# Kernel optimization log

Hardware: AMD Instinct MI355X
Metric: run time of the kernel (lower is better)

The kernel has to match this reference:

```python
import jax, jax.numpy as jnp
import numpy as np

N_HEAD = 8
D_MODEL = 128  # per-head dim == d_model in this 'interpretable' MHA
B, S = 2, 2048
LN_EPS = 1e-3  # keras LayerNormalization default epsilon


def setup_inputs() -> dict:
    key = jax.random.key(0)
    ks = jax.random.split(key, 8)
    sc = 1.0 / np.sqrt(D_MODEL)
    q = jax.random.normal(ks[0], (B, S, D_MODEL), jnp.float32)
    k = jax.random.normal(ks[1], (B, S, D_MODEL), jnp.float32)
    v = jax.random.normal(ks[2], (B, S, D_MODEL), jnp.float32)
    # multiplicative causal mask (lower-triangular ones), broadcast over B,H
    mask = jnp.tril(jnp.ones((S, S), jnp.float32))[None, None, :, :]
    Wq = jax.random.normal(ks[3], (D_MODEL, N_HEAD * D_MODEL), jnp.float32) * sc
    Wk = jax.random.normal(ks[4], (D_MODEL, N_HEAD * D_MODEL), jnp.float32) * sc
    Wv = jax.random.normal(ks[5], (D_MODEL, N_HEAD * D_MODEL), jnp.float32) * sc
    Wo = jax.random.normal(ks[6], (N_HEAD * D_MODEL, D_MODEL), jnp.float32) * sc
    gamma = jnp.ones((D_MODEL,), jnp.float32)
    beta = jnp.zeros((D_MODEL,), jnp.float32)
    return {"q": q, "k": k, "v": v, "mask": mask, "Wq": Wq, "Wk": Wk,
            "Wv": Wv, "Wo": Wo, "gamma": gamma, "beta": beta}


def reference(q, k, v, mask, Wq, Wk, Wv, Wo, gamma, beta):
    b = q.shape[0]
    # projections -> [B, H, S, D]
    def split_heads(x):
        return x.reshape(b, -1, N_HEAD, D_MODEL).transpose(0, 2, 1, 3)
    qs = split_heads(q @ Wq)
    ks_ = split_heads(k @ Wk)
    vs = split_heads(v @ Wv)
    scores = jnp.einsum('bhqd,bhkd->bhqk', qs, ks_) / jnp.sqrt(jnp.float32(D_MODEL))
    scores = scores * mask  # multiplicative mask (NOT additive -inf)
    attn = jax.nn.softmax(scores, axis=-1)
    # dropout layers are identity at inference
    out = jnp.einsum('bhqk,bhkd->bhqd', attn, vs)
    out = out.transpose(0, 2, 1, 3).reshape(b, -1, N_HEAD * D_MODEL)
    out = out @ Wo
    # keras LayerNorm (axis=-1, eps=1e-3)
    mu = jnp.mean(out, axis=-1, keepdims=True)
    var = jnp.var(out, axis=-1, keepdims=True)
    out = (out - mu) * jax.lax.rsqrt(var + LN_EPS) * gamma + beta
    return out
```

## Files before the change

### kernel.cpp

```cpp
#include <hip/hip_runtime.h>
#include <math.h>

#define B 2
#define S 2048
#define H 8
#define D 128
#define DM 1024
#define BH 16

typedef unsigned short u16;
typedef __attribute__((ext_vector_type(8))) short bf16x8;
typedef __attribute__((ext_vector_type(8))) unsigned short u16x8;
typedef __attribute__((ext_vector_type(4))) float f32x4;

__device__ __forceinline__ float bf2f(u16 x) {
    union { unsigned u; float f; } c; c.u = ((unsigned)x) << 16; return c.f;
}
__device__ __forceinline__ u16 f2bf(float f) {
    union { unsigned u; float f; } c; c.f = f;
    unsigned u = c.u; u += 0x7fffu + ((u >> 16) & 1u);
    return (u16)(u >> 16);
}
__device__ __forceinline__ u16 ftr(float f) {
    union { unsigned u; float f; } c; c.f = f;
    return (u16)(c.u >> 16);
}

#define MFMA16(a, b, c) __builtin_amdgcn_mfma_f32_16x16x32_bf16((a), (b), (c), 0, 0, 0)

__global__ __launch_bounds__(256) void prep_kernel(
    const float* __restrict__ Wq, const float* __restrict__ Wk, const float* __restrict__ Wv,
    const float* __restrict__ Wo, u16* __restrict__ WT, u16* __restrict__ WoT)
{
    __shared__ __align__(16) u16 Wl[128][132];
    int tid = threadIdx.x, by = blockIdx.x;
    if (by < 16) {
        int k0 = by * 64;
#pragma unroll
        for (int i = 0; i < 8; i++) {
            int e = i * 256 + tid; int kk = e >> 5, n4 = e & 31;
            float4 w4 = *(const float4*)&Wo[(size_t)(k0 + kk) * D + n4 * 4];
            ushort4 p; p.x = ftr(w4.x); p.y = ftr(w4.y); p.z = ftr(w4.z); p.w = ftr(w4.w);
            *(ushort4*)&Wl[kk][n4 * 4] = p;
        }
        __syncthreads();
#pragma unroll
        for (int i = 0; i < 4; i++) {
            int e = i * 256 + tid; int n = e >> 3, ko = e & 7;
            u16x8 g;
#pragma unroll
            for (int j = 0; j < 8; j++) g[j] = Wl[ko * 8 + j][n];
            *(u16x8*)&WoT[(size_t)n * DM + k0 + ko * 8] = g;
        }
    } else {
        int tile = by - 16;
        int t = tile >> 3, h = tile & 7;
        const float* W = (t == 0) ? Wq : (t == 1) ? Wk : Wv;
        int col0 = h * 128;
#pragma unroll
        for (int i = 0; i < 16; i++) {
            int e = i * 256 + tid; int kk = e >> 5, n4 = e & 31;
            float4 w4 = *(const float4*)&W[(size_t)kk * DM + col0 + n4 * 4];
            ushort4 p; p.x = ftr(w4.x); p.y = ftr(w4.y); p.z = ftr(w4.z); p.w = ftr(w4.w);
            *(ushort4*)&Wl[kk][n4 * 4] = p;
        }
        __syncthreads();
        u16* WTt = WT + (size_t)tile * (128 * 128);
#pragma unroll
        for (int i = 0; i < 8; i++) {
            int e = i * 256 + tid; int n = e >> 4, ko = e & 15;
            u16x8 g;
#pragma unroll
            for (int j = 0; j < 8; j++) g[j] = Wl[ko * 8 + j][n];
            *(u16x8*)&WTt[(size_t)n * 128 + ko * 8] = g;
        }
    }
}

__global__ __launch_bounds__(256) void proj_kernel(
    const float* __restrict__ q, const float* __restrict__ k, const float* __restrict__ v,
    const u16* __restrict__ WT,
    u16* __restrict__ Qo, u16* __restrict__ Ko, u16* __restrict__ VTo,
    float* __restrict__ Csum)
{
    __shared__ __align__(16) u16 Xs[128][136];
    int tid = threadIdx.x;
    int m0 = blockIdx.x * 128;
    int by = blockIdx.y;
    int t = by >> 3;
    int h = by & 7;
    const float* X = (t == 0) ? q : (t == 1) ? k : v;
    const u16* WTt = WT + (size_t)(t * 8 + h) * (128 * 128);

#pragma unroll
    for (int i = 0; i < 16; i++) {
        int e = i * 256 + tid; int r = e >> 5, c4 = e & 31;
        float4 x4 = *(const float4*)&X[(size_t)(m0 + r) * D + c4 * 4];
        ushort4 p; p.x = ftr(x4.x); p.y = ftr(x4.y); p.z = ftr(x4.z); p.w = ftr(x4.w);
        *(ushort4*)&Xs[r][c4 * 4] = p;
    }
    __syncthreads();

    int w = tid >> 6, lane = tid & 63, quad = lane >> 4, ln = lane & 15;
    bf16x8 aX[2][4];
#pragma unroll
    for (int rf = 0; rf < 2; rf++)
#pragma unroll
        for (int ks = 0; ks < 4; ks++)
            aX[rf][ks] = *(const bf16x8*)&Xs[w * 32 + rf * 16 + ln][ks * 32 + quad * 8];

    f32x4 zero = {0.f, 0.f, 0.f, 0.f};
    f32x4 acc[2][8];
#pragma unroll
    for (int rf = 0; rf < 2; rf++)
#pragma unroll
        for (int nt = 0; nt < 8; nt++) acc[rf][nt] = zero;

#pragma unroll
    for (int ks = 0; ks < 4; ks++) {
        bf16x8 bW[8];
#pragma unroll
        for (int nt = 0; nt < 8; nt++)
            bW[nt] = *(const bf16x8*)&WTt[(size_t)(nt * 16 + ln) * 128 + ks * 32 + quad * 8];
#pragma unroll
        for (int nt = 0; nt < 8; nt++) {
            acc[0][nt] = MFMA16(aX[0][ks], bW[nt], acc[0][nt]);
            acc[1][nt] = MFMA16(aX[1][ks], bW[nt], acc[1][nt]);
        }
    }

    int bb = m0 >> 11, ss0 = m0 & 2047;
    int bh = bb * 8 + h;
    if (t < 2) {
        u16* O = (t == 0) ? Qo : Ko;
#pragma unroll
        for (int rf = 0; rf < 2; rf++)
#pragma unroll
            for (int nt = 0; nt < 8; nt++)
#pragma unroll
                for (int r = 0; r < 4; r++) {
                    int ss = ss0 + w * 32 + rf * 16 + quad * 4 + r;
                    O[((size_t)bh * S + ss) * D + nt * 16 + ln] = f2bf(acc[rf][nt][r]);
                }
    } else {
        __syncthreads();
        u16 (*Ct)[136] = Xs;
#pragma unroll
        for (int rf = 0; rf < 2; rf++)
#pragma unroll
            for (int nt = 0; nt < 8; nt++)
#pragma unroll
                for (int r = 0; r < 4; r++)
                    Ct[nt * 16 + ln][w * 32 + rf * 16 + quad * 4 + r] = f2bf(acc[rf][nt][r]);
        __syncthreads();
#pragma unroll
        for (int i = 0; i < 8; i++) {
            int e = i * 256 + tid; int dloc = e >> 4, s8 = e & 15;
            *(u16x8*)&VTo[((size_t)bh * D + dloc) * S + ss0 + s8 * 8] =
                *(const u16x8*)&Ct[dloc][s8 * 8];
        }
        {
            int d = tid >> 1, c = tid & 1;
            float s = 0.f;
#pragma unroll
            for (int i = 0; i < 8; i++) {
                u16x8 v8 = *(const u16x8*)&Ct[d][c * 64 + i * 8];
#pragma unroll
                for (int j = 0; j < 8; j++) s += bf2f(v8[j]);
            }
            Csum[((size_t)bh * 32 + (ss0 >> 6) + c) * D + d] = s;
        }
    }
}

__global__ __launch_bounds__(128) void scan_kernel(
    const float* __restrict__ Csum, float* __restrict__ SufT)
{
    int bh = blockIdx.x, d = threadIdx.x;
    float acc = 0.f;
    for (int c = 31; c >= 0; c--) {
        SufT[((size_t)bh * 32 + c) * D + d] = acc;
        acc += Csum[((size_t)bh * 32 + c) * D + d];
    }
}

__global__ __launch_bounds__(512, 2) void attn_kernel(
    const u16* __restrict__ Qb, const u16* __restrict__ Kb, const u16* __restrict__ VTg,
    const float* __restrict__ SufT, u16* __restrict__ HOb)
{
    __shared__ __align__(16) u16 Qs[2][64][136];
    __shared__ __align__(16) u16 Ks[128][136];
    __shared__ __align__(16) u16 Vt[128][136];
    __shared__ __align__(16) u16 Ps[2][64][136];
    __shared__ float Lred[2][4][64];

    int tid = threadIdx.x;
    int bx = blockIdx.x, bh = blockIdx.y;
    int nhi = (31 - bx) / 2 + 1, nlo = bx / 2 + 1;
    int w = tid >> 6, qt = w >> 2, wq = w & 3, lane = tid & 63, quad = lane >> 4, ln = lane & 15;
    int qb = qt ? bx : (31 - bx);
    int q0 = qb * 64;
    int nq = qt ? nlo : nhi;
    const u16* Qp  = Qb  + (size_t)bh * S * D;
    const u16* Kp  = Kb  + (size_t)bh * S * D;
    const u16* VTp = VTg + (size_t)bh * D * S;

#pragma unroll
    for (int i = 0; i < 4; i++) {
        int e = i * 512 + tid; int r2 = e >> 4, c8 = e & 15;
        int qtt = r2 >> 6, r = r2 & 63;
        int q0s = (qtt ? bx : (31 - bx)) * 64;
        *(u16x8*)&Qs[qtt][r][c8 * 8] = *(const u16x8*)&Qp[(size_t)(q0s + r) * D + c8 * 8];
    }
    __syncthreads();
    bf16x8 aQ[4][4];
#pragma unroll
    for (int rf = 0; rf < 4; rf++)
#pragma unroll
        for (int ks = 0; ks < 4; ks++)
            aQ[rf][ks] = *(const bf16x8*)&Qs[qt][rf * 16 + ln][ks * 32 + quad * 8];

    f32x4 zero = {0.f, 0.f, 0.f, 0.f};
    f32x4 accPV[4][2], acc_l[4];
#pragma unroll
    for (int rf = 0; rf < 4; rf++) { accPV[rf][0] = zero; accPV[rf][1] = zero; acc_l[rf] = zero; }
    bf16x8 bOnes;
#pragma unroll
    for (int j = 0; j < 8; j++) bOnes[j] = (short)0x3F80;
    const float scale = 0.08838834764831845f;

    for (int kt = 0; kt < nhi; kt++) {
        __syncthreads();
        int k0 = kt * 128;
#pragma unroll
        for (int i = 0; i < 4; i++) {
            int e = i * 512 + tid; int r = e >> 4, c8 = e & 15;
            *(u16x8*)&Ks[r][c8 * 8] = *(const u16x8*)&Kp[(size_t)(k0 + r) * D + c8 * 8];
        }
#pragma unroll
        for (int i = 0; i < 4; i++) {
            int e = i * 512 + tid; int dd = e >> 4, c8 = e & 15;
            *(u16x8*)&Vt[dd][c8 * 8] = *(const u16x8*)&VTp[(size_t)dd * S + k0 + c8 * 8];
        }
        __syncthreads();
        bool active = (qt == 0) || (kt < nlo);
        if (active) {
            f32x4 s[4][2];
#pragma unroll
            for (int rf = 0; rf < 4; rf++) { s[rf][0] = zero; s[rf][1] = zero; }
#pragma unroll
            for (int ks = 0; ks < 4; ks++) {
                bf16x8 b0 = *(const bf16x8*)&Ks[wq * 32 + ln][ks * 32 + quad * 8];
                bf16x8 b1 = *(const bf16x8*)&Ks[wq * 32 + 16 + ln][ks * 32 + quad * 8];
#pragma unroll
                for (int rf = 0; rf < 4; rf++) {
                    s[rf][0] = MFMA16(aQ[rf][ks], b0, s[rf][0]);
                    s[rf][1] = MFMA16(aQ[rf][ks], b1, s[rf][1]);
                }
            }
#pragma unroll
            for (int rf = 0; rf < 4; rf++)
#pragma unroll
                for (int ct = 0; ct < 2; ct++) {
                    int col = k0 + wq * 32 + ct * 16 + ln;
                    int rowb = q0 + rf * 16 + quad * 4;
#pragma unroll
                    for (int r = 0; r < 4; r++) {
                        float tv = (col <= rowb + r) ? s[rf][ct][r] : 0.f;
                        float p = __expf(tv * scale);
                        Ps[qt][rf * 16 + quad * 4 + r][wq * 32 + ct * 16 + ln] = f2bf(p);
                    }
                }
        }
        __syncthreads();
        if (active) {
#pragma unroll
            for (int ks = 0; ks < 4; ks++) {
                bf16x8 aP[4];
#pragma unroll
                for (int rf = 0; rf < 4; rf++)
                    aP[rf] = *(const bf16x8*)&Ps[qt][rf * 16 + ln][ks * 32 + quad * 8];
                bf16x8 v0 = *(const bf16x8*)&Vt[wq * 32 + ln][ks * 32 + quad * 8];
                bf16x8 v1 = *(const bf16x8*)&Vt[wq * 32 + 16 + ln][ks * 32 + quad * 8];
                if (ks == wq) {
#pragma unroll
                    for (int rf = 0; rf < 4; rf++) acc_l[rf] = MFMA16(aP[rf], bOnes, acc_l[rf]);
                }
#pragma unroll
                for (int rf = 0; rf < 4; rf++) {
                    accPV[rf][0] = MFMA16(aP[rf], v0, accPV[rf][0]);
                    accPV[rf][1] = MFMA16(aP[rf], v1, accPV[rf][1]);
                }
            }
        }
    }

    __syncthreads();
    if (ln == 0) {
#pragma unroll
        for (int rf = 0; rf < 4; rf++)
#pragma unroll
            for (int r = 0; r < 4; r++)
                Lred[qt][wq][rf * 16 + quad * 4 + r] = acc_l[rf][r];
    }
    __syncthreads();

    int scount = S - nq * 128;
    size_t sufb = (size_t)(bh * 32 + 2 * nq - 1) * D + wq * 32;
    float suf0 = SufT[sufb + ln];
    float suf1 = SufT[sufb + 16 + ln];
    int b = bh >> 3, h = bh & 7;
#pragma unroll
    for (int rf = 0; rf < 4; rf++)
#pragma unroll
        for (int r = 0; r < 4; r++) {
            int row = rf * 16 + quad * 4 + r;
            int srow = q0 + row;
            float l = Lred[qt][0][row] + Lred[qt][1][row] + Lred[qt][2][row] + Lred[qt][3][row]
                      + (float)scount;
            float inv = 1.f / l;
            size_t base = ((size_t)(b * S + srow)) * DM + h * D + wq * 32;
            HOb[base + ln]      = f2bf((accPV[rf][0][r] + suf0) * inv);
            HOb[base + 16 + ln] = f2bf((accPV[rf][1][r] + suf1) * inv);
        }
}

__global__ __launch_bounds__(256) void out_ln_kernel(
    const u16* __restrict__ HOb, const u16* __restrict__ WoT,
    const float* __restrict__ gamma, const float* __restrict__ beta,
    float* __restrict__ out)
{
    __shared__ __align__(16) u16 HOs[16][1048];
    __shared__ float Cs[16][132];
    int tid = threadIdx.x;
    int m0 = blockIdx.x * 16;
    int w = tid >> 6, lane = tid & 63, quad = lane >> 4, ln = lane & 15;
#pragma unroll
    for (int i = 0; i < 8; i++) {
        int e = i * 256 + tid; int r = e >> 7, c8 = e & 127;
        *(u16x8*)&HOs[r][c8 * 8] = *(const u16x8*)&HOb[(size_t)(m0 + r) * DM + c8 * 8];
    }
    __syncthreads();
    f32x4 zero = {0.f, 0.f, 0.f, 0.f};
    f32x4 acc[2] = {zero, zero};
#pragma unroll 4
    for (int ks = 0; ks < 32; ks++) {
        bf16x8 aH = *(const bf16x8*)&HOs[ln][ks * 32 + quad * 8];
        bf16x8 w0 = *(const bf16x8*)&WoT[(size_t)(w * 32 + ln) * DM + ks * 32 + quad * 8];
        bf16x8 w1 = *(const bf16x8*)&WoT[(size_t)(w * 32 + 16 + ln) * DM + ks * 32 + quad * 8];
        acc[0] = MFMA16(aH, w0, acc[0]);
        acc[1] = MFMA16(aH, w1, acc[1]);
    }
#pragma unroll
    for (int ct = 0; ct < 2; ct++)
#pragma unroll
        for (int r = 0; r < 4; r++)
            Cs[quad * 4 + r][w * 32 + ct * 16 + ln] = acc[ct][r];
    __syncthreads();

    int row = tid >> 4, t16 = tid & 15;
    float xv[8], sum = 0.f, sq = 0.f;
#pragma unroll
    for (int j = 0; j < 8; j++) {
        float x = Cs[row][t16 * 8 + j];
        xv[j] = x; sum += x; sq += x * x;
    }
#pragma unroll
    for (int off = 1; off < 16; off <<= 1) {
        sum += __shfl_xor(sum, off);
        sq  += __shfl_xor(sq, off);
    }
    float mu = sum * (1.f / 128.f);
    float var = sq * (1.f / 128.f) - mu * mu;
    float rstd = rsqrtf(var + 1e-3f);
    float o[8];
#pragma unroll
    for (int j = 0; j < 8; j++) {
        int c = t16 * 8 + j;
        o[j] = (xv[j] - mu) * rstd * gamma[c] + beta[c];
    }
    float* op = &out[(size_t)(m0 + row) * D + t16 * 8];
    *(float4*)&op[0] = *(float4*)&o[0];
    *(float4*)&op[4] = *(float4*)&o[4];
}

extern "C" void kernel_launch(void* const* d_in, const int* in_sizes, int n_in,
                              void* d_out, int out_size, void* d_ws, size_t ws_size,
                              hipStream_t stream)
{
    const float* q     = (const float*)d_in[0];
    const float* k     = (const float*)d_in[1];
    const float* v     = (const float*)d_in[2];
    const float* Wq    = (const float*)d_in[4];
    const float* Wk    = (const float*)d_in[5];
    const float* Wv    = (const float*)d_in[6];
    const float* Wo    = (const float*)d_in[7];
    const float* gamma = (const float*)d_in[8];
    const float* beta  = (const float*)d_in[9];

    u16* ws16 = (u16*)d_ws;
    u16* Qb  = ws16;
    u16* Kb  = ws16 + 4194304;
    u16* VT  = ws16 + 8388608;
    u16* HOb = ws16 + 12582912;
    u16* WoT = ws16 + 16777216;
    u16* WT  = ws16 + 16908288;
    float* Csum = (float*)((char*)d_ws + 35651584);
    float* SufT = (float*)((char*)d_ws + 35913728);

    prep_kernel<<<40, 256, 0, stream>>>(Wq, Wk, Wv, Wo, WT, WoT);
    proj_kernel<<<dim3(32, 24), 256, 0, stream>>>(q, k, v, WT, Qb, Kb, VT, Csum);
    scan_kernel<<<BH, 128, 0, stream>>>(Csum, SufT);
    attn_kernel<<<dim3(16, BH), 512, 0, stream>>>(Qb, Kb, VT, SufT, HOb);
    out_ln_kernel<<<256, 256, 0, stream>>>(HOb, WoT, gamma, beta, (float*)d_out);
}
```

Before: 165.4 us.

## Restructure attention to one 64-row query tile per block and drop scan kernel

The attention kernel now gives each block a single 64-row query tile with 4 waves of 16 rows and 64-key tiles. This replaces the paired high/low tile scheme that used 512 threads. The grid doubles to 512 blocks, each block loads only the key tiles it needs, and the suffix sum over masked value chunks is computed inline from Csum, which removes the separate scan kernel launch. The projection kernel stages the weight tile in LDS and writes Q/K through LDS with coalesced 16-byte stores. Costs are redundant suffix summation per thread and more K/V tile reloads across blocks.

```diff
diff --git a/kernel.cpp b/kernel.cpp
--- a/kernel.cpp
+++ b/kernel.cpp
@@ -84,6 +84,7 @@
     float* __restrict__ Csum)
 {
     __shared__ __align__(16) u16 Xs[128][136];
+    __shared__ __align__(16) u16 Ws[128][136];
     int tid = threadIdx.x;
     int m0 = blockIdx.x * 128;
     int by = blockIdx.y;
@@ -99,6 +100,11 @@
         ushort4 p; p.x = ftr(x4.x); p.y = ftr(x4.y); p.z = ftr(x4.z); p.w = ftr(x4.w);
         *(ushort4*)&Xs[r][c4 * 4] = p;
     }
+#pragma unroll
+    for (int i = 0; i < 8; i++) {
+        int e = i * 256 + tid; int n = e >> 4, c8 = e & 15;
+        *(u16x8*)&Ws[n][c8 * 8] = *(const u16x8*)&WTt[(size_t)n * 128 + c8 * 8];
+    }
     __syncthreads();
 
     int w = tid >> 6, lane = tid & 63, quad = lane >> 4, ln = lane & 15;
@@ -121,7 +127,7 @@
         bf16x8 bW[8];
 #pragma unroll
         for (int nt = 0; nt < 8; nt++)
-            bW[nt] = *(const bf16x8*)&WTt[(size_t)(nt * 16 + ln) * 128 + ks * 32 + quad * 8];
+            bW[nt] = *(const bf16x8*)&Ws[nt * 16 + ln][ks * 32 + quad * 8];
 #pragma unroll
         for (int nt = 0; nt < 8; nt++) {
             acc[0][nt] = MFMA16(aX[0][ks], bW[nt], acc[0][nt]);
@@ -131,6 +137,8 @@
 
     int bb = m0 >> 11, ss0 = m0 & 2047;
     int bh = bb * 8 + h;
+    __syncthreads();
+    u16 (*Ct)[136] = Xs;
     if (t < 2) {
         u16* O = (t == 0) ? Qo : Ko;
 #pragma unroll
@@ -138,13 +146,15 @@
 #pragma unroll
             for (int nt = 0; nt < 8; nt++)
 #pragma unroll
-                for (int r = 0; r < 4; r++) {
-                    int ss = ss0 + w * 32 + rf * 16 + quad * 4 + r;
-                    O[((size_t)bh * S + ss) * D + nt * 16 + ln] = f2bf(acc[rf][nt][r]);
-                }
+                for (int r = 0; r < 4; r++)
+                    Ct[w * 32 + rf * 16 + quad * 4 + r][nt * 16 + ln] = f2bf(acc[rf][nt][r]);
+        __syncthreads();
+#pragma unroll
+        for (int i = 0; i < 8; i++) {
+            int e = i * 256 + tid; int r = e >> 4, c8 = e & 15;
+            *(u16x8*)&O[((size_t)bh * S + ss0 + r) * D + c8 * 8] = *(const u16x8*)&Ct[r][c8 * 8];
+        }
     } else {
-        __syncthreads();
-        u16 (*Ct)[136] = Xs;
 #pragma unroll
         for (int rf = 0; rf < 2; rf++)
 #pragma unroll
@@ -173,156 +183,105 @@
     }
 }
 
-__global__ __launch_bounds__(128) void scan_kernel(
-    const float* __restrict__ Csum, float* __restrict__ SufT)
-{
-    int bh = blockIdx.x, d = threadIdx.x;
-    float acc = 0.f;
-    for (int c = 31; c >= 0; c--) {
-        SufT[((size_t)bh * 32 + c) * D + d] = acc;
-        acc += Csum[((size_t)bh * 32 + c) * D + d];
-    }
-}
-
-__global__ __launch_bounds__(512, 2) void attn_kernel(
+__global__ __launch_bounds__(256, 3) void attn_kernel(
     const u16* __restrict__ Qb, const u16* __restrict__ Kb, const u16* __restrict__ VTg,
-    const float* __restrict__ SufT, u16* __restrict__ HOb)
-{
-    __shared__ __align__(16) u16 Qs[2][64][136];
-    __shared__ __align__(16) u16 Ks[128][136];
-    __shared__ __align__(16) u16 Vt[128][136];
-    __shared__ __align__(16) u16 Ps[2][64][136];
-    __shared__ float Lred[2][4][64];
+    const float* __restrict__ Csum, u16* __restrict__ HOb)
+{
+    __shared__ __align__(16) u16 Ks[64][136];
+    __shared__ __align__(16) u16 Vt[128][72];
+    __shared__ __align__(16) u16 Ps[4][16][72];
 
     int tid = threadIdx.x;
-    int bx = blockIdx.x, bh = blockIdx.y;
-    int nhi = (31 - bx) / 2 + 1, nlo = bx / 2 + 1;
-    int w = tid >> 6, qt = w >> 2, wq = w & 3, lane = tid & 63, quad = lane >> 4, ln = lane & 15;
-    int qb = qt ? bx : (31 - bx);
+    int qb = 31 - blockIdx.x;
+    int bh = blockIdx.y;
     int q0 = qb * 64;
-    int nq = qt ? nlo : nhi;
+    int nt = (qb & ~1) + 2;
+    int w = tid >> 6, lane = tid & 63, quad = lane >> 4, ln = lane & 15;
     const u16* Qp  = Qb  + (size_t)bh * S * D;
     const u16* Kp  = Kb  + (size_t)bh * S * D;
     const u16* VTp = VTg + (size_t)bh * D * S;
 
-#pragma unroll
-    for (int i = 0; i < 4; i++) {
-        int e = i * 512 + tid; int r2 = e >> 4, c8 = e & 15;
-        int qtt = r2 >> 6, r = r2 & 63;
-        int q0s = (qtt ? bx : (31 - bx)) * 64;
-        *(u16x8*)&Qs[qtt][r][c8 * 8] = *(const u16x8*)&Qp[(size_t)(q0s + r) * D + c8 * 8];
-    }
-    __syncthreads();
-    bf16x8 aQ[4][4];
-#pragma unroll
-    for (int rf = 0; rf < 4; rf++)
-#pragma unroll
-        for (int ks = 0; ks < 4; ks++)
-            aQ[rf][ks] = *(const bf16x8*)&Qs[qt][rf * 16 + ln][ks * 32 + quad * 8];
+    bf16x8 aQ[4];
+    int qrow = q0 + w * 16 + ln;
+#pragma unroll
+    for (int ks = 0; ks < 4; ks++)
+        aQ[ks] = *(const bf16x8*)&Qp[(size_t)qrow * D + ks * 32 + quad * 8];
 
     f32x4 zero = {0.f, 0.f, 0.f, 0.f};
-    f32x4 accPV[4][2], acc_l[4];
-#pragma unroll
-    for (int rf = 0; rf < 4; rf++) { accPV[rf][0] = zero; accPV[rf][1] = zero; acc_l[rf] = zero; }
+    f32x4 accPV[8], acc_l[4];
+#pragma unroll
+    for (int jd = 0; jd < 8; jd++) accPV[jd] = zero;
+#pragma unroll
+    for (int g = 0; g < 4; g++) acc_l[g] = zero;
     bf16x8 bOnes;
 #pragma unroll
     for (int j = 0; j < 8; j++) bOnes[j] = (short)0x3F80;
     const float scale = 0.08838834764831845f;
 
-    for (int kt = 0; kt < nhi; kt++) {
-        __syncthreads();
-        int k0 = kt * 128;
+    for (int kt = 0; kt < nt; kt++) {
+        __syncthreads();
+        int k0 = kt * 64;
 #pragma unroll
         for (int i = 0; i < 4; i++) {
-            int e = i * 512 + tid; int r = e >> 4, c8 = e & 15;
+            int e = i * 256 + tid; int r = e >> 4, c8 = e & 15;
             *(u16x8*)&Ks[r][c8 * 8] = *(const u16x8*)&Kp[(size_t)(k0 + r) * D + c8 * 8];
         }
 #pragma unroll
         for (int i = 0; i < 4; i++) {
-            int e = i * 512 + tid; int dd = e >> 4, c8 = e & 15;
+            int e = i * 256 + tid; int dd = e >> 3, c8 = e & 7;
             *(u16x8*)&Vt[dd][c8 * 8] = *(const u16x8*)&VTp[(size_t)dd * S + k0 + c8 * 8];
         }
         __syncthreads();
-        bool active = (qt == 0) || (kt < nlo);
-        if (active) {
-            f32x4 s[4][2];
-#pragma unroll
-            for (int rf = 0; rf < 4; rf++) { s[rf][0] = zero; s[rf][1] = zero; }
+
+#pragma unroll
+        for (int ct = 0; ct < 4; ct++) {
+            f32x4 s = zero;
 #pragma unroll
             for (int ks = 0; ks < 4; ks++) {
-                bf16x8 b0 = *(const bf16x8*)&Ks[wq * 32 + ln][ks * 32 + quad * 8];
-                bf16x8 b1 = *(const bf16x8*)&Ks[wq * 32 + 16 + ln][ks * 32 + quad * 8];
-#pragma unroll
-                for (int rf = 0; rf < 4; rf++) {
-                    s[rf][0] = MFMA16(aQ[rf][ks], b0, s[rf][0]);
-                    s[rf][1] = MFMA16(aQ[rf][ks], b1, s[rf][1]);
-                }
+                bf16x8 bK = *(const bf16x8*)&Ks[ct * 16 + ln][ks * 32 + quad * 8];
+                s = MFMA16(aQ[ks], bK, s);
             }
-#pragma unroll
-            for (int rf = 0; rf < 4; rf++)
-#pragma unroll
-                for (int ct = 0; ct < 2; ct++) {
-                    int col = k0 + wq * 32 + ct * 16 + ln;
-                    int rowb = q0 + rf * 16 + quad * 4;
-#pragma unroll
-                    for (int r = 0; r < 4; r++) {
-                        float tv = (col <= rowb + r) ? s[rf][ct][r] : 0.f;
-                        float p = __expf(tv * scale);
-                        Ps[qt][rf * 16 + quad * 4 + r][wq * 32 + ct * 16 + ln] = f2bf(p);
-                    }
-                }
-        }
-        __syncthreads();
-        if (active) {
-#pragma unroll
-            for (int ks = 0; ks < 4; ks++) {
-                bf16x8 aP[4];
-#pragma unroll
-                for (int rf = 0; rf < 4; rf++)
-                    aP[rf] = *(const bf16x8*)&Ps[qt][rf * 16 + ln][ks * 32 + quad * 8];
-                bf16x8 v0 = *(const bf16x8*)&Vt[wq * 32 + ln][ks * 32 + quad * 8];
-                bf16x8 v1 = *(const bf16x8*)&Vt[wq * 32 + 16 + ln][ks * 32 + quad * 8];
-                if (ks == wq) {
-#pragma unroll
-                    for (int rf = 0; rf < 4; rf++) acc_l[rf] = MFMA16(aP[rf], bOnes, acc_l[rf]);
-                }
-#pragma unroll
-                for (int rf = 0; rf < 4; rf++) {
-                    accPV[rf][0] = MFMA16(aP[rf], v0, accPV[rf][0]);
-                    accPV[rf][1] = MFMA16(aP[rf], v1, accPV[rf][1]);
-                }
+            int col = k0 + ct * 16 + ln;
+            int rowb = q0 + w * 16 + quad * 4;
+#pragma unroll
+            for (int r = 0; r < 4; r++) {
+                float tv = (col <= rowb + r) ? s[r] : 0.f;
+                Ps[w][quad * 4 + r][ct * 16 + ln] = f2bf(__expf(tv * scale));
             }
         }
-    }
-
-    __syncthreads();
-    if (ln == 0) {
-#pragma unroll
-        for (int rf = 0; rf < 4; rf++)
-#pragma unroll
-            for (int r = 0; r < 4; r++)
-                Lred[qt][wq][rf * 16 + quad * 4 + r] = acc_l[rf][r];
-    }
-    __syncthreads();
-
-    int scount = S - nq * 128;
-    size_t sufb = (size_t)(bh * 32 + 2 * nq - 1) * D + wq * 32;
-    float suf0 = SufT[sufb + ln];
-    float suf1 = SufT[sufb + 16 + ln];
+#pragma unroll
+        for (int ks = 0; ks < 2; ks++) {
+            bf16x8 aP = *(const bf16x8*)&Ps[w][ln][ks * 32 + quad * 8];
+            int g = (2 * kt + ks) & 3;
+            acc_l[g] = MFMA16(aP, bOnes, acc_l[g]);
+#pragma unroll
+            for (int jd = 0; jd < 8; jd++) {
+                bf16x8 vf = *(const bf16x8*)&Vt[jd * 16 + ln][ks * 32 + quad * 8];
+                accPV[jd] = MFMA16(aP, vf, accPV[jd]);
+            }
+        }
+    }
+
+    float suf[8];
+#pragma unroll
+    for (int jd = 0; jd < 8; jd++) suf[jd] = 0.f;
+    for (int c = 31; c >= nt; c--) {
+        const float* cp = &Csum[((size_t)(bh * 32 + c)) * D + ln];
+#pragma unroll
+        for (int jd = 0; jd < 8; jd++) suf[jd] += cp[jd * 16];
+    }
+    int scount = S - nt * 64;
     int b = bh >> 3, h = bh & 7;
 #pragma unroll
-    for (int rf = 0; rf < 4; rf++)
-#pragma unroll
-        for (int r = 0; r < 4; r++) {
-            int row = rf * 16 + quad * 4 + r;
-            int srow = q0 + row;
-            float l = Lred[qt][0][row] + Lred[qt][1][row] + Lred[qt][2][row] + Lred[qt][3][row]
-                      + (float)scount;
-            float inv = 1.f / l;
-            size_t base = ((size_t)(b * S + srow)) * DM + h * D + wq * 32;
-            HOb[base + ln]      = f2bf((accPV[rf][0][r] + suf0) * inv);
-            HOb[base + 16 + ln] = f2bf((accPV[rf][1][r] + suf1) * inv);
-        }
+    for (int r = 0; r < 4; r++) {
+        int srow = q0 + w * 16 + quad * 4 + r;
+        float l = ((acc_l[0][r] + acc_l[1][r]) + acc_l[2][r]) + acc_l[3][r] + (float)scount;
+        float inv = 1.f / l;
+        size_t base = ((size_t)(b * S + srow)) * DM + h * D;
+#pragma unroll
+        for (int jd = 0; jd < 8; jd++)
+            HOb[base + jd * 16 + ln] = f2bf((accPV[jd][r] + suf[jd]) * inv);
+    }
 }
 
 __global__ __launch_bounds__(256) void out_ln_kernel(
@@ -406,11 +365,9 @@
     u16* WoT = ws16 + 16777216;
     u16* WT  = ws16 + 16908288;
     float* Csum = (float*)((char*)d_ws + 35651584);
-    float* SufT = (float*)((char*)d_ws + 35913728);
 
     prep_kernel<<<40, 256, 0, stream>>>(Wq, Wk, Wv, Wo, WT, WoT);
     proj_kernel<<<dim3(32, 24), 256, 0, stream>>>(q, k, v, WT, Qb, Kb, VT, Csum);
-    scan_kernel<<<BH, 128, 0, stream>>>(Csum, SufT);
-    attn_kernel<<<dim3(16, BH), 512, 0, stream>>>(Qb, Kb, VT, SufT, HOb);
+    attn_kernel<<<dim3(32, BH), 256, 0, stream>>>(Qb, Kb, VT, Csum, HOb);
     out_ln_kernel<<<256, 256, 0, stream>>>(HOb, WoT, gamma, beta, (float*)d_out);
 }
```

Measured after the change: 178.4 us. 1.08x slower.
